# Optimization experiments

Hardware: AMD Instinct MI355X
Metric: run time of the kernel (lower is better)

## Reference

```python
import jax, jax.numpy as jnp
import numpy as np

B, N, D, H, DA, DL = 8, 1024, 512, 8, 64, 64
DFF = 4 * D
EPS = 1e-6


def layer_norm(x, g, b):
    mu = jnp.mean(x, axis=-1, keepdims=True)
    var = jnp.mean(jnp.square(x - mu), axis=-1, keepdims=True)
    return (x - mu) * jax.lax.rsqrt(var + EPS) * g + b


def setup_inputs() -> dict:
    key = jax.random.key(0)
    ks = jax.random.split(key, 12)
    T = B * N
    x = jax.random.normal(ks[0], (T, D), dtype=jnp.float32)
    x_offsets = (jnp.arange(B + 1, dtype=jnp.int64) * N)
    invalid_attn_mask = jnp.tril(jnp.ones((N, N), dtype=jnp.float32))  # causal
    s = lambda fin: 1.0 / np.sqrt(fin)
    W_q = jax.random.normal(ks[1], (D, H * DA), jnp.float32) * s(D)
    b_q = jnp.zeros((H * DA,), jnp.float32)
    W_k = jax.random.normal(ks[2], (D, H * DA), jnp.float32) * s(D)
    b_k = jnp.zeros((H * DA,), jnp.float32)
    W_v = jax.random.normal(ks[3], (D, H * DL), jnp.float32) * s(D)
    b_v = jnp.zeros((H * DL,), jnp.float32)
    W_o = jax.random.normal(ks[4], (H * DL, D), jnp.float32) * s(H * DL)
    b_o = jnp.zeros((D,), jnp.float32)
    ln1_g = jnp.ones((D,), jnp.float32); ln1_b = jnp.zeros((D,), jnp.float32)
    ln2_g = jnp.ones((D,), jnp.float32); ln2_b = jnp.zeros((D,), jnp.float32)
    W_f1 = jax.random.normal(ks[5], (D, DFF), jnp.float32) * s(D)
    b_f1 = jnp.zeros((DFF,), jnp.float32)
    W_f2 = jax.random.normal(ks[6], (DFF, D), jnp.float32) * s(DFF)
    b_f2 = jnp.zeros((D,), jnp.float32)
    return dict(x=x, x_offsets=x_offsets, invalid_attn_mask=invalid_attn_mask,
                W_q=W_q, b_q=b_q, W_k=W_k, b_k=b_k, W_v=W_v, b_v=b_v,
                W_o=W_o, b_o=b_o, ln1_g=ln1_g, ln1_b=ln1_b, ln2_g=ln2_g,
                ln2_b=ln2_b, W_f1=W_f1, b_f1=b_f1, W_f2=W_f2, b_f2=b_f2)


def reference(x, x_offsets, invalid_attn_mask, W_q, b_q, W_k, b_k, W_v, b_v,
              W_o, b_o, ln1_g, ln1_b, ln2_g, ln2_b, W_f1, b_f1, W_f2, b_f2):
    T = x.shape[0]
    n = invalid_attn_mask.shape[-1]
    h = layer_norm(x, ln1_g, ln1_b)
    q = h @ W_q + b_q  # [T, H*DA]
    k = h @ W_k + b_k
    v = h @ W_v + b_v  # [T, H*DL]
    # jagged -> dense padding (vectorized)
    lengths = x_offsets[1:] - x_offsets[:-1]          # [B]
    pos = jnp.arange(n)
    idx = x_offsets[:-1, None] + pos[None, :]          # [B, n] flat token index
    valid = pos[None, :] < jnp.minimum(lengths, n)[:, None]
    idx_c = jnp.clip(idx, 0, T - 1)
    pq = jnp.where(valid[..., None], q[idx_c], 0.0).reshape(B, n, H, DA)
    pk = jnp.where(valid[..., None], k[idx_c], 0.0).reshape(B, n, H, DA)
    pv = jnp.where(valid[..., None], v[idx_c], 0.0).reshape(B, n, H, DL)
    scores = jnp.einsum('bnhd,bmhd->bhnm', pq, pk) / np.sqrt(DA)
    scores = jnp.where(invalid_attn_mask[None, None] == 0, -jnp.inf, scores)
    attn = jax.nn.softmax(scores, axis=-1)            # [B, H, n, n]
    out = jnp.einsum('bhnm,bmhd->bnhd', attn, pv).reshape(B, n, H * DL)
    # dense -> jagged unpadding (assumes all lengths <= n, as in setup)
    t = jnp.arange(T)
    b_idx = jnp.searchsorted(x_offsets, t, side='right') - 1
    p_idx = t - x_offsets[b_idx]
    attn_j = out[b_idx, p_idx]                         # [T, H*DL]
    x = x + (attn_j @ W_o + b_o)
    h2 = layer_norm(x, ln2_g, ln2_b)
    ffn = jax.nn.silu(h2 @ W_f1 + b_f1) @ W_f2 + b_f2
    return x + ffn
```

## Files before the change

kernel.cpp:

```cpp
#include <hip/hip_runtime.h>


typedef __bf16 bf16x8 __attribute__((ext_vector_type(8)));
typedef float f32x4 __attribute__((ext_vector_type(4)));

#define GLOAD16(g, l)                                                      \
  __builtin_amdgcn_global_load_lds(                                       \
      (const __attribute__((address_space(1))) void*)(g),                 \
      (__attribute__((address_space(3))) void*)(l), 16, 0, 0)

#define WAITVM(N) asm volatile("s_waitcnt vmcnt(" #N ")" ::: "memory")
#define WAITLGKM0 asm volatile("s_waitcnt lgkmcnt(0)" ::: "memory")
#define BAR() __builtin_amdgcn_s_barrier()

__global__ __launch_bounds__(256) void prep_kernel(
    const float* __restrict__ Wq, const float* __restrict__ Wk,
    const float* __restrict__ Wv, const float* __restrict__ Wo,
    const float* __restrict__ Wf1, const float* __restrict__ Wf2,
    const float* __restrict__ bq, const float* __restrict__ bk,
    const float* __restrict__ bv, __bf16* __restrict__ wqkv,
    __bf16* __restrict__ wo_t, __bf16* __restrict__ wf1_t,
    __bf16* __restrict__ wf2_t, float* __restrict__ bqkv) {
  __shared__ float t[32][33];
  const int id = blockIdx.x;
  if (id >= 3072) {
    int i = (id - 3072) * 256 + threadIdx.x;
    float v;
    if (i < 512) v = bq[i];
    else if (i < 1024) v = bk[i - 512];
    else v = bv[i - 1024];
    bqkv[i] = v;
    return;
  }
  const float* src;
  __bf16* dst;
  int K, N, bx, by;
  if (id < 1024) {
    const int which = id >> 8, tt = id & 255;
    bx = tt & 15;
    by = tt >> 4;
    K = 512;
    N = 512;
    if (which == 0) { src = Wq; dst = wqkv; }
    else if (which == 1) { src = Wk; dst = wqkv + 512 * 512; }
    else if (which == 2) { src = Wv; dst = wqkv + 1024 * 512; }
    else { src = Wo; dst = wo_t; }
  } else if (id < 2048) {
    const int tt = id - 1024;
    bx = tt & 63;
    by = tt >> 6;
    K = 512;
    N = 2048;
    src = Wf1;
    dst = wf1_t;
  } else {
    const int tt = id - 2048;
    bx = tt & 15;
    by = tt >> 4;
    K = 2048;
    N = 512;
    src = Wf2;
    dst = wf2_t;
  }
  const int n0 = bx * 32, k0 = by * 32;
  const int tx = threadIdx.x & 31, ty = threadIdx.x >> 5;
#pragma unroll
  for (int i = 0; i < 4; i++)
    t[ty + i * 8][tx] = src[(size_t)(k0 + ty + i * 8) * N + n0 + tx];
  __syncthreads();
#pragma unroll
  for (int i = 0; i < 4; i++)
    dst[(size_t)(n0 + ty + i * 8) * K + k0 + tx] = (__bf16)t[tx][ty + i * 8];
}

__global__ __launch_bounds__(256) void ln_kernel(const float* __restrict__ x,
                                                 const float* __restrict__ g,
                                                 const float* __restrict__ bta,
                                                 __bf16* __restrict__ out) {
  const int row = blockIdx.x * 4 + (threadIdx.x >> 6);
  const int lane = threadIdx.x & 63;
  const float4* xr = (const float4*)(x + (size_t)row * 512);
  float4 v0 = xr[lane * 2 + 0];
  float4 v1 = xr[lane * 2 + 1];
  float s = v0.x + v0.y + v0.z + v0.w + v1.x + v1.y + v1.z + v1.w;
  float sq = v0.x * v0.x + v0.y * v0.y + v0.z * v0.z + v0.w * v0.w +
             v1.x * v1.x + v1.y * v1.y + v1.z * v1.z + v1.w * v1.w;
#pragma unroll
  for (int o = 1; o < 64; o <<= 1) {
    s += __shfl_xor(s, o);
    sq += __shfl_xor(sq, o);
  }
  const float mu = s * (1.0f / 512.0f);
  const float var = sq * (1.0f / 512.0f) - mu * mu;
  const float rs = rsqrtf(var + 1e-6f);
  const float4* gr = (const float4*)g + lane * 2;
  const float4* br = (const float4*)bta + lane * 2;
  float4 g0 = gr[0], g1 = gr[1], b0 = br[0], b1 = br[1];
  bf16x8 o8;
  o8[0] = (__bf16)((v0.x - mu) * rs * g0.x + b0.x);
  o8[1] = (__bf16)((v0.y - mu) * rs * g0.y + b0.y);
  o8[2] = (__bf16)((v0.z - mu) * rs * g0.z + b0.z);
  o8[3] = (__bf16)((v0.w - mu) * rs * g0.w + b0.w);
  o8[4] = (__bf16)((v1.x - mu) * rs * g1.x + b1.x);
  o8[5] = (__bf16)((v1.y - mu) * rs * g1.y + b1.y);
  o8[6] = (__bf16)((v1.z - mu) * rs * g1.z + b1.z);
  o8[7] = (__bf16)((v1.w - mu) * rs * g1.w + b1.w);
  *(bf16x8*)(out + (size_t)row * 512 + lane * 8) = o8;
}

template <int EPI>
__global__ __launch_bounds__(256) void gemm_bt(
    const __bf16* __restrict__ A, const __bf16* __restrict__ Bt,
    const float* __restrict__ bias, const float* __restrict__ resid,
    void* __restrict__ outp, int M, int N, int K) {
  __shared__ __bf16 As[2][128 * 32];
  __shared__ __bf16 Bs[2][128 * 32];
  const int tid = threadIdx.x;
  const int lane = tid & 63;
  const int w = tid >> 6;
  const int brow = blockIdx.x * 128;
  const int bcol = blockIdx.y * 128;

  f32x4 acc[4][4] = {};

  const int srow = tid >> 2;
  const int sc = (tid & 3) ^ (srow & 3);
  const __bf16* a_src = A + (size_t)(brow + srow) * K + sc * 8;
  const __bf16* b_src = Bt + (size_t)(bcol + srow) * K + sc * 8;

  const int wr = w >> 1, wc = w & 1;
  const int lr = lane & 15, lg = lane >> 4;
  const int arow = wr * 64 + lr;
  const int brf = wc * 64 + lr;
  const int sw = ((lg ^ (lr & 3)) << 3);

#define STAGE128(buf, koff)                                                 \
  do {                                                                      \
    GLOAD16(a_src + (koff), &As[buf][w * 512]);                             \
    GLOAD16(a_src + (size_t)64 * K + (koff), &As[buf][2048 + w * 512]);     \
    GLOAD16(b_src + (koff), &Bs[buf][w * 512]);                             \
    GLOAD16(b_src + (size_t)64 * K + (koff), &Bs[buf][2048 + w * 512]);     \
  } while (0)

  const int T = K >> 5;
  STAGE128(0, 0);
  STAGE128(1, 32);

  for (int t = 0; t < T; ++t) {
    if (t + 1 < T) WAITVM(4);
    else WAITVM(0);
    BAR();
    const int cur = t & 1;
    bf16x8 af[4], bfv[4];
#pragma unroll
    for (int m = 0; m < 4; m++)
      af[m] = *(const bf16x8*)&As[cur][(arow + m * 16) * 32 + sw];
#pragma unroll
    for (int n = 0; n < 4; n++)
      bfv[n] = *(const bf16x8*)&Bs[cur][(brf + n * 16) * 32 + sw];
    WAITLGKM0;
    BAR();
    if (t + 2 < T) STAGE128(cur, (t + 2) * 32);
    __builtin_amdgcn_s_setprio(1);
#pragma unroll
    for (int m = 0; m < 4; m++)
#pragma unroll
      for (int n = 0; n < 4; n++)
        acc[m][n] =
            __builtin_amdgcn_mfma_f32_16x16x32_bf16(af[m], bfv[n], acc[m][n], 0, 0, 0);
    __builtin_amdgcn_s_setprio(0);
  }
#undef STAGE128

  const int rbase = brow + wr * 64 + (lg << 2);
  const int cbase = bcol + wc * 64 + lr;
#pragma unroll
  for (int m = 0; m < 4; m++) {
#pragma unroll
    for (int n = 0; n < 4; n++) {
      const int col = cbase + n * 16;
      const float bv = bias[col];
#pragma unroll
      for (int j = 0; j < 4; j++) {
        const int row = rbase + m * 16 + j;
        float v = acc[m][n][j] + bv;
        const size_t idx = (size_t)row * N + col;
        if (EPI == 0) {
          ((__bf16*)outp)[idx] = (__bf16)v;
        } else if (EPI == 1) {
          ((__bf16*)outp)[idx] = (__bf16)(v / (1.0f + __expf(-v)));
        } else if (EPI == 2) {
          ((float*)outp)[idx] = v + resid[idx];
        } else {
          ((float*)outp)[idx] += v;
        }
      }
    }
  }
}

template <int EPI>
__global__ __launch_bounds__(256) void gemm_bt_n64(
    const __bf16* __restrict__ A, const __bf16* __restrict__ Bt,
    const float* __restrict__ bias, const float* __restrict__ resid,
    void* __restrict__ outp, int M, int N, int K) {
  __shared__ __bf16 As[2][128 * 64];
  __shared__ __bf16 Bs[2][64 * 64];
  const int tid = threadIdx.x;
  const int lane = tid & 63;
  const int w = tid >> 6;
  const int brow = blockIdx.x * 128;
  const int bcol = blockIdx.y * 64;

  f32x4 acc[2][4] = {};

  const int srow = tid >> 3;
  const int sc = (tid & 7) ^ (srow & 7);
  const __bf16* a_src = A + (size_t)(brow + srow) * K + sc * 8;
  const __bf16* b_src = Bt + (size_t)(bcol + srow) * K + sc * 8;

  const int lr = lane & 15, lg = lane >> 4;
  const int arow0 = w * 32 + lr;
  const int sw0 = ((lg ^ (lr & 7)) << 3);

#define STAGE_N64(buf, koff)                                               \
  do {                                                                     \
    GLOAD16(a_src + (koff), &As[buf][w * 512]);                            \
    GLOAD16(a_src + (size_t)32 * K + (koff), &As[buf][2048 + w * 512]);    \
    GLOAD16(a_src + (size_t)64 * K + (koff), &As[buf][4096 + w * 512]);    \
    GLOAD16(a_src + (size_t)96 * K + (koff), &As[buf][6144 + w * 512]);    \
    GLOAD16(b_src + (koff), &Bs[buf][w * 512]);                            \
    GLOAD16(b_src + (size_t)32 * K + (koff), &Bs[buf][2048 + w * 512]);    \
  } while (0)

  const int T = K >> 6;
  STAGE_N64(0, 0);
  STAGE_N64(1, 64);

  for (int t = 0; t < T; ++t) {
    if (t + 1 < T) WAITVM(6);
    else WAITVM(0);
    BAR();
    const int cur = t & 1;
    bf16x8 af[2][2], bfv[4][2];
#pragma unroll
    for (int m = 0; m < 2; m++) {
      const int r = (arow0 + m * 16) * 64;
      af[m][0] = *(const bf16x8*)&As[cur][r + sw0];
      af[m][1] = *(const bf16x8*)&As[cur][r + (sw0 ^ 32)];
    }
#pragma unroll
    for (int n = 0; n < 4; n++) {
      const int r = (n * 16 + lr) * 64;
      bfv[n][0] = *(const bf16x8*)&Bs[cur][r + sw0];
      bfv[n][1] = *(const bf16x8*)&Bs[cur][r + (sw0 ^ 32)];
    }
    WAITLGKM0;
    BAR();
    if (t + 2 < T) STAGE_N64(cur, (t + 2) * 64);
    __builtin_amdgcn_s_setprio(1);
#pragma unroll
    for (int m = 0; m < 2; m++)
#pragma unroll
      for (int n = 0; n < 4; n++)
#pragma unroll
        for (int s = 0; s < 2; s++)
          acc[m][n] = __builtin_amdgcn_mfma_f32_16x16x32_bf16(
              af[m][s], bfv[n][s], acc[m][n], 0, 0, 0);
    __builtin_amdgcn_s_setprio(0);
  }
#undef STAGE_N64

  const int rbase = brow + w * 32 + (lg << 2);
  const int cbase = bcol + lr;
#pragma unroll
  for (int m = 0; m < 2; m++) {
#pragma unroll
    for (int n = 0; n < 4; n++) {
      const int col = cbase + n * 16;
      const float bv = bias[col];
#pragma unroll
      for (int j = 0; j < 4; j++) {
        const int row = rbase + m * 16 + j;
        float v = acc[m][n][j] + bv;
        const size_t idx = (size_t)row * N + col;
        if (EPI == 0) {
          ((__bf16*)outp)[idx] = (__bf16)v;
        } else if (EPI == 1) {
          ((__bf16*)outp)[idx] = (__bf16)(v / (1.0f + __expf(-v)));
        } else if (EPI == 2) {
          ((float*)outp)[idx] = v + resid[idx];
        } else {
          ((float*)outp)[idx] += v;
        }
      }
    }
  }
}

__global__ __launch_bounds__(256) void vtrans_kernel(
    const __bf16* __restrict__ qkv, __bf16* __restrict__ vt) {
  const int bh = blockIdx.y, b = bh >> 3, h = bh & 7;
  const int n0 = blockIdx.x * 64;
  __shared__ __bf16 t[64][72];
  const int tx = threadIdx.x & 3, ty = threadIdx.x >> 2;
  const __bf16* src =
      qkv + (size_t)(b * 1024 + n0 + ty) * 1536 + 1024 + h * 64 + tx * 16;
  bf16x8 v0 = *(const bf16x8*)(src);
  bf16x8 v1 = *(const bf16x8*)(src + 8);
  *(bf16x8*)&t[ty][tx * 16] = v0;
  *(bf16x8*)&t[ty][tx * 16 + 8] = v1;
  __syncthreads();
  bf16x8 o0, o1;
#pragma unroll
  for (int j = 0; j < 8; j++) {
    o0[j] = t[tx * 16 + j][ty];
    o1[j] = t[tx * 16 + 8 + j][ty];
  }
  __bf16* dst = vt + (size_t)(bh * 64 + ty) * 1024 + n0 + tx * 16;
  *(bf16x8*)dst = o0;
  *(bf16x8*)(dst + 8) = o1;
}

__global__ __launch_bounds__(256) void attn_kernel(
    const __bf16* __restrict__ qkv, const __bf16* __restrict__ vt,
    __bf16* __restrict__ out) {
  const int bid = blockIdx.x;
  const int qb = 15 - (bid >> 6);
  const int bh = bid & 63;
  const int b = bh >> 3, h = bh & 7;
  const int tid = threadIdx.x;
  const int lane = tid & 63, w = tid >> 6;
  const int qr = qb * 64 + w * 16;
  const int lr = lane & 15, lg = lane >> 4;

  __shared__ __bf16 Ks[2][64 * 64];
  __shared__ __bf16 Vs[2][64 * 64];
  __shared__ __bf16 Plds[4][16][72];

  const __bf16* Qp = qkv + (size_t)b * 1024 * 1536 + h * 64;
  const __bf16* Kp = Qp + 512;
  const __bf16* Vp = vt + (size_t)bh * 64 * 1024;

  const int srow = tid >> 3;
  const int kc = (tid & 7) ^ (srow & 7);
  const __bf16* ksrcA = Kp + (size_t)srow * 1536 + kc * 8;
  const __bf16* ksrcB = Kp + (size_t)(srow + 32) * 1536 + kc * 8;
  const __bf16* vsrcA = Vp + (size_t)srow * 1024 + kc * 8;
  const __bf16* vsrcB = Vp + (size_t)(srow + 32) * 1024 + kc * 8;

#define STAGE_ATT(buf, nb)                                                 \
  do {                                                                     \
    GLOAD16(ksrcA + (size_t)(nb) * 1536, &Ks[buf][w * 512]);               \
    GLOAD16(ksrcB + (size_t)(nb) * 1536, &Ks[buf][2048 + w * 512]);        \
    GLOAD16(vsrcA + (nb), &Vs[buf][w * 512]);                              \
    GLOAD16(vsrcB + (nb), &Vs[buf][2048 + w * 512]);                       \
  } while (0)

  bf16x8 qf[2];
#pragma unroll
  for (int s = 0; s < 2; s++)
    qf[s] = *(const bf16x8*)(Qp + (size_t)(qr + lr) * 1536 + s * 32 + lg * 8);

  f32x4 accO[4] = {};
  float m_run[4], l_run[4];
#pragma unroll
  for (int j = 0; j < 4; j++) {
    m_run[j] = -1e30f;
    l_run[j] = 0.f;
  }

  STAGE_ATT(0, 0);
  if (qb >= 1) STAGE_ATT(1, 64);

  for (int kt = 0; kt <= qb; ++kt) {
    const int kb = kt * 64;
    const int cur = kt & 1;
    if (kt < qb) WAITVM(4);
    else WAITVM(0);
    BAR();
    f32x4 sa[4] = {};
    __builtin_amdgcn_s_setprio(1);
#pragma unroll
    for (int n = 0; n < 4; n++) {
      const int row = n * 16 + lr;
#pragma unroll
      for (int s = 0; s < 2; s++) {
        bf16x8 kf = *(const bf16x8*)&Ks[cur][row * 64 +
                                             (((s * 4 + lg) ^ (row & 7)) << 3)];
        sa[n] = __builtin_amdgcn_mfma_f32_16x16x32_bf16(qf[s], kf, sa[n], 0, 0, 0);
      }
    }
    __builtin_amdgcn_s_setprio(0);
    const bool domask = (kt == qb);
    float corr[4];
#pragma unroll
    for (int j = 0; j < 4; j++) {
      const int row = qr + lg * 4 + j;
      float mx = -1e30f;
#pragma unroll
      for (int n = 0; n < 4; n++) {
        float v = sa[n][j] * 0.125f;
        if (domask && (kb + n * 16 + lr) > row) v = -1e30f;
        sa[n][j] = v;
        mx = fmaxf(mx, v);
      }
#pragma unroll
      for (int o = 1; o < 16; o <<= 1) mx = fmaxf(mx, __shfl_xor(mx, o));
      const float mnew = fmaxf(m_run[j], mx);
      corr[j] = __expf(m_run[j] - mnew);
      m_run[j] = mnew;
      float ps = 0.f;
#pragma unroll
      for (int n = 0; n < 4; n++) {
        float p = __expf(sa[n][j] - mnew);
        sa[n][j] = p;
        ps += p;
      }
#pragma unroll
      for (int o = 1; o < 16; o <<= 1) ps += __shfl_xor(ps, o);
      l_run[j] = l_run[j] * corr[j] + ps;
    }
#pragma unroll
    for (int n = 0; n < 4; n++)
#pragma unroll
      for (int j = 0; j < 4; j++) accO[n][j] *= corr[j];
#pragma unroll
    for (int n = 0; n < 4; n++)
#pragma unroll
      for (int j = 0; j < 4; j++)
        Plds[w][lg * 4 + j][n * 16 + lr] = (__bf16)sa[n][j];
    __builtin_amdgcn_s_setprio(1);
#pragma unroll
    for (int s = 0; s < 2; s++) {
      bf16x8 pf = *(const bf16x8*)&Plds[w][lr][s * 32 + lg * 8];
#pragma unroll
      for (int n = 0; n < 4; n++) {
        const int row = n * 16 + lr;
        bf16x8 vf = *(const bf16x8*)&Vs[cur][row * 64 +
                                             (((s * 4 + lg) ^ (row & 7)) << 3)];
        accO[n] = __builtin_amdgcn_mfma_f32_16x16x32_bf16(pf, vf, accO[n], 0, 0, 0);
      }
    }
    __builtin_amdgcn_s_setprio(0);
    WAITLGKM0;
    BAR();
    if (kt + 2 <= qb) STAGE_ATT(cur, (kt + 2) * 64);
  }
#undef STAGE_ATT

#pragma unroll
  for (int n = 0; n < 4; n++) {
#pragma unroll
    for (int j = 0; j < 4; j++) {
      const int row = qr + lg * 4 + j;
      const float v = accO[n][j] / l_run[j];
      out[(size_t)(b * 1024 + row) * 512 + h * 64 + n * 16 + lr] = (__bf16)v;
    }
  }
}

extern "C" void kernel_launch(void* const* d_in, const int* in_sizes, int n_in,
                              void* d_out, int out_size, void* d_ws,
                              size_t ws_size, hipStream_t stream) {
  const float* x = (const float*)d_in[0];
  const float* Wq = (const float*)d_in[3];
  const float* bq = (const float*)d_in[4];
  const float* Wk = (const float*)d_in[5];
  const float* bk = (const float*)d_in[6];
  const float* Wv = (const float*)d_in[7];
  const float* bv = (const float*)d_in[8];
  const float* Wo = (const float*)d_in[9];
  const float* bo = (const float*)d_in[10];
  const float* ln1g = (const float*)d_in[11];
  const float* ln1b = (const float*)d_in[12];
  const float* ln2g = (const float*)d_in[13];
  const float* ln2b = (const float*)d_in[14];
  const float* Wf1 = (const float*)d_in[15];
  const float* bf1 = (const float*)d_in[16];
  const float* Wf2 = (const float*)d_in[17];
  const float* bf2 = (const float*)d_in[18];
  float* out = (float*)d_out;

  char* ws = (char*)d_ws;
  if (ws_size < 65018880ULL) return;
  __bf16* h1 = (__bf16*)(ws + 0);
  __bf16* h2 = (__bf16*)(ws + 8388608);
  __bf16* attn = (__bf16*)(ws + 16777216);
  __bf16* wqkv = (__bf16*)(ws + 25165824);
  __bf16* wo_t = (__bf16*)(ws + 26738688);
  __bf16* wf1_t = (__bf16*)(ws + 27262976);
  __bf16* wf2_t = (__bf16*)(ws + 29360128);
  float* bqkv = (float*)(ws + 31457280);
  __bf16* qkv = (__bf16*)(ws + 31464448);
  __bf16* vt = (__bf16*)(ws + 56630272);
  __bf16* ffn1 = qkv;

  prep_kernel<<<3078, 256, 0, stream>>>(Wq, Wk, Wv, Wo, Wf1, Wf2, bq, bk, bv,
                                        wqkv, wo_t, wf1_t, wf2_t, bqkv);

  ln_kernel<<<2048, 256, 0, stream>>>(x, ln1g, ln1b, h1);
  gemm_bt<0><<<dim3(64, 12), 256, 0, stream>>>(h1, wqkv, bqkv, nullptr, qkv,
                                               8192, 1536, 512);
  vtrans_kernel<<<dim3(16, 64), 256, 0, stream>>>(qkv, vt);
  attn_kernel<<<1024, 256, 0, stream>>>(qkv, vt, attn);
  gemm_bt_n64<2><<<dim3(64, 8), 256, 0, stream>>>(attn, wo_t, bo, x, out, 8192,
                                                  512, 512);
  ln_kernel<<<2048, 256, 0, stream>>>(out, ln2g, ln2b, h2);
  gemm_bt<1><<<dim3(64, 16), 256, 0, stream>>>(h2, wf1_t, bf1, nullptr, ffn1,
                                               8192, 2048, 512);
  gemm_bt_n64<3><<<dim3(64, 8), 256, 0, stream>>>(ffn1, wf2_t, bf2, nullptr,
                                                  out, 8192, 512, 2048);
}
```

Measured before the change: 150.3 us.

## Replace 128x128 GEMM with 256x256 tile, 512-thread kernel for QKV and FFN1

Replaces the 128x128-tile, BK=32 GEMM used for the QKV projection and the FFN up-projection with a 256x256-tile, BK=64 kernel using 8 waves. Each wave computes a 128x64 sub-tile in four phases. The goal is more data reuse per byte loaded and fewer loop iterations. The cost is 128KB of LDS per block and fewer blocks (192 and 256). That may underfill the 256 CUs, and the pipeline now waits on vmcnt(0) each iteration, so less load latency is hidden.

```diff
diff --git a/kernel.cpp b/kernel.cpp
--- a/kernel.cpp
+++ b/kernel.cpp
@@ -109,73 +109,83 @@
 }
 
 template <int EPI>
-__global__ __launch_bounds__(256) void gemm_bt(
+__global__ __launch_bounds__(512) void gemm256(
     const __bf16* __restrict__ A, const __bf16* __restrict__ Bt,
-    const float* __restrict__ bias, const float* __restrict__ resid,
-    void* __restrict__ outp, int M, int N, int K) {
-  __shared__ __bf16 As[2][128 * 32];
-  __shared__ __bf16 Bs[2][128 * 32];
+    const float* __restrict__ bias, __bf16* __restrict__ outp, int M, int N,
+    int K) {
+  __shared__ __bf16 As[2][256 * 64];
+  __shared__ __bf16 Bs[2][256 * 64];
   const int tid = threadIdx.x;
-  const int lane = tid & 63;
-  const int w = tid >> 6;
-  const int brow = blockIdx.x * 128;
-  const int bcol = blockIdx.y * 128;
-
-  f32x4 acc[4][4] = {};
-
-  const int srow = tid >> 2;
-  const int sc = (tid & 3) ^ (srow & 3);
+  const int lane = tid & 63, w = tid >> 6;
+  const int wr = w >> 2, wc = w & 3;
+  const int lr = lane & 15, lg = lane >> 4;
+  const int brow = blockIdx.x * 256;
+  const int bcol = blockIdx.y * 256;
+
+  f32x4 acc[8][4] = {};
+
+  const int srow = tid >> 3;
+  const int sc = (tid & 7) ^ (srow & 7);
   const __bf16* a_src = A + (size_t)(brow + srow) * K + sc * 8;
   const __bf16* b_src = Bt + (size_t)(bcol + srow) * K + sc * 8;
 
-  const int wr = w >> 1, wc = w & 1;
-  const int lr = lane & 15, lg = lane >> 4;
-  const int arow = wr * 64 + lr;
-  const int brf = wc * 64 + lr;
-  const int sw = ((lg ^ (lr & 3)) << 3);
-
-#define STAGE128(buf, koff)                                                 \
-  do {                                                                      \
-    GLOAD16(a_src + (koff), &As[buf][w * 512]);                             \
-    GLOAD16(a_src + (size_t)64 * K + (koff), &As[buf][2048 + w * 512]);     \
-    GLOAD16(b_src + (koff), &Bs[buf][w * 512]);                             \
-    GLOAD16(b_src + (size_t)64 * K + (koff), &Bs[buf][2048 + w * 512]);     \
+#define STAGE256(buf, koff)                                                \
+  do {                                                                     \
+    _Pragma("unroll") for (int i = 0; i < 4; i++)                          \
+        GLOAD16(a_src + (size_t)(i * 64) * K + (koff),                     \
+                &As[buf][w * 512 + i * 4096]);                             \
+    _Pragma("unroll") for (int i = 0; i < 4; i++)                          \
+        GLOAD16(b_src + (size_t)(i * 64) * K + (koff),                     \
+                &Bs[buf][w * 512 + i * 4096]);                             \
   } while (0)
 
-  const int T = K >> 5;
-  STAGE128(0, 0);
-  STAGE128(1, 32);
-
+  const int T = K >> 6;
+  STAGE256(0, 0);
+
+  int cur = 0;
   for (int t = 0; t < T; ++t) {
-    if (t + 1 < T) WAITVM(4);
-    else WAITVM(0);
+    WAITVM(0);
     BAR();
-    const int cur = t & 1;
-    bf16x8 af[4], bfv[4];
-#pragma unroll
-    for (int m = 0; m < 4; m++)
-      af[m] = *(const bf16x8*)&As[cur][(arow + m * 16) * 32 + sw];
-#pragma unroll
-    for (int n = 0; n < 4; n++)
-      bfv[n] = *(const bf16x8*)&Bs[cur][(brf + n * 16) * 32 + sw];
-    WAITLGKM0;
-    BAR();
-    if (t + 2 < T) STAGE128(cur, (t + 2) * 32);
-    __builtin_amdgcn_s_setprio(1);
-#pragma unroll
-    for (int m = 0; m < 4; m++)
-#pragma unroll
-      for (int n = 0; n < 4; n++)
-        acc[m][n] =
-            __builtin_amdgcn_mfma_f32_16x16x32_bf16(af[m], bfv[n], acc[m][n], 0, 0, 0);
-    __builtin_amdgcn_s_setprio(0);
-  }
-#undef STAGE128
-
-  const int rbase = brow + wr * 64 + (lg << 2);
+    if (t + 1 < T) STAGE256(cur ^ 1, (t + 1) * 64);
+#pragma unroll
+    for (int ph = 0; ph < 4; ++ph) {
+      const int mh = ph >> 1, nh = ph & 1;
+      bf16x8 af[4][2], bfv[2][2];
+#pragma unroll
+      for (int mm = 0; mm < 4; mm++) {
+        const int row = wr * 128 + (mh * 4 + mm) * 16 + lr;
+#pragma unroll
+        for (int s = 0; s < 2; s++)
+          af[mm][s] =
+              *(const bf16x8*)&As[cur][row * 64 + (((s * 4 + lg) ^ (lr & 7)) << 3)];
+      }
+#pragma unroll
+      for (int nn = 0; nn < 2; nn++) {
+        const int row = wc * 64 + (nh * 2 + nn) * 16 + lr;
+#pragma unroll
+        for (int s = 0; s < 2; s++)
+          bfv[nn][s] =
+              *(const bf16x8*)&Bs[cur][row * 64 + (((s * 4 + lg) ^ (lr & 7)) << 3)];
+      }
+      __builtin_amdgcn_s_setprio(1);
+#pragma unroll
+      for (int mm = 0; mm < 4; mm++)
+#pragma unroll
+        for (int nn = 0; nn < 2; nn++)
+#pragma unroll
+          for (int s = 0; s < 2; s++)
+            acc[mh * 4 + mm][nh * 2 + nn] = __builtin_amdgcn_mfma_f32_16x16x32_bf16(
+                af[mm][s], bfv[nn][s], acc[mh * 4 + mm][nh * 2 + nn], 0, 0, 0);
+      __builtin_amdgcn_s_setprio(0);
+    }
+    cur ^= 1;
+  }
+#undef STAGE256
+
+  const int rbase = brow + wr * 128 + (lg << 2);
   const int cbase = bcol + wc * 64 + lr;
 #pragma unroll
-  for (int m = 0; m < 4; m++) {
+  for (int m = 0; m < 8; m++) {
 #pragma unroll
     for (int n = 0; n < 4; n++) {
       const int col = cbase + n * 16;
@@ -184,16 +194,8 @@
       for (int j = 0; j < 4; j++) {
         const int row = rbase + m * 16 + j;
         float v = acc[m][n][j] + bv;
-        const size_t idx = (size_t)row * N + col;
-        if (EPI == 0) {
-          ((__bf16*)outp)[idx] = (__bf16)v;
-        } else if (EPI == 1) {
-          ((__bf16*)outp)[idx] = (__bf16)(v / (1.0f + __expf(-v)));
-        } else if (EPI == 2) {
-          ((float*)outp)[idx] = v + resid[idx];
-        } else {
-          ((float*)outp)[idx] += v;
-        }
+        if (EPI == 1) v = v / (1.0f + __expf(-v));
+        outp[(size_t)row * N + col] = (__bf16)v;
       }
     }
   }
@@ -284,11 +286,7 @@
         const int row = rbase + m * 16 + j;
         float v = acc[m][n][j] + bv;
         const size_t idx = (size_t)row * N + col;
-        if (EPI == 0) {
-          ((__bf16*)outp)[idx] = (__bf16)v;
-        } else if (EPI == 1) {
-          ((__bf16*)outp)[idx] = (__bf16)(v / (1.0f + __expf(-v)));
-        } else if (EPI == 2) {
+        if (EPI == 2) {
           ((float*)outp)[idx] = v + resid[idx];
         } else {
           ((float*)outp)[idx] += v;
@@ -500,15 +498,15 @@
                                         wqkv, wo_t, wf1_t, wf2_t, bqkv);
 
   ln_kernel<<<2048, 256, 0, stream>>>(x, ln1g, ln1b, h1);
-  gemm_bt<0><<<dim3(64, 12), 256, 0, stream>>>(h1, wqkv, bqkv, nullptr, qkv,
-                                               8192, 1536, 512);
+  gemm256<0><<<dim3(32, 6), 512, 0, stream>>>(h1, wqkv, bqkv, qkv, 8192, 1536,
+                                              512);
   vtrans_kernel<<<dim3(16, 64), 256, 0, stream>>>(qkv, vt);
   attn_kernel<<<1024, 256, 0, stream>>>(qkv, vt, attn);
   gemm_bt_n64<2><<<dim3(64, 8), 256, 0, stream>>>(attn, wo_t, bo, x, out, 8192,
                                                   512, 512);
   ln_kernel<<<2048, 256, 0, stream>>>(out, ln2g, ln2b, h2);
-  gemm_bt<1><<<dim3(64, 16), 256, 0, stream>>>(h2, wf1_t, bf1, nullptr, ffn1,
-                                               8192, 2048, 512);
+  gemm256<1><<<dim3(32, 8), 512, 0, stream>>>(h2, wf1_t, bf1, ffn1, 8192, 2048,
+                                              512);
   gemm_bt_n64<3><<<dim3(64, 8), 256, 0, stream>>>(ffn1, wf2_t, bf2, nullptr,
                                                   out, 8192, 512, 2048);
 }
```

New measurement: 152.9 us. No clear change (+1.7%).
